# Performance work log

Hardware: AMD Instinct MI355X
Metric: run time of the kernel (lower is better)

Reference implementation:

```python
import jax, jax.numpy as jnp
import numpy as np

E = 8           # num_experts
K = 2           # num_experts_per_tok
D = 1024        # hidden_size
F = 2048        # intermediate_dim
B, S = 1, 2048  # batch, seq_len


def setup_inputs() -> dict:
    key = jax.random.key(0)
    k0, k1, k2, k3, k4, k5 = jax.random.split(key, 6)
    hidden_states = jax.random.normal(k0, (B, S, D), dtype=jnp.float32)
    topk_weights = jax.random.uniform(k1, (B * S, K), dtype=jnp.float32)
    topk_ids = jax.random.randint(k2, (B * S, K), 0, E, dtype=jnp.int32)
    scale = 0.02
    wi_0 = jax.random.normal(k3, (E, D, F), dtype=jnp.float32) * scale
    wi_1 = jax.random.normal(k4, (E, D, F), dtype=jnp.float32) * scale
    wo = jax.random.normal(k5, (E, F, D), dtype=jnp.float32) * scale
    return {"hidden_states": hidden_states, "topk_weights": topk_weights,
            "topk_ids": topk_ids, "wi_0": wi_0, "wi_1": wi_1, "wo": wo}


def _gmm(x, w, group_sizes):
    """Grouped matmul: rows of x are sorted by expert; group_sizes[e] rows use w[e].
    Small fixed loop over experts (E=8); rows not owned by expert e are masked out."""
    n_e = w.shape[0]
    expert_of_row = jnp.repeat(jnp.arange(n_e), group_sizes,
                               total_repeat_length=x.shape[0])  # [M]
    out = jnp.zeros((x.shape[0], w.shape[2]), dtype=x.dtype)
    for e in range(n_e):
        out = out + jnp.where((expert_of_row == e)[:, None], x @ w[e], 0.0)
    return out


def _moe_forward(hidden_states, topk_weights, topk_ids, wi_0, wi_1, wo):
    b, s, d = hidden_states.shape
    k = topk_ids.shape[1]
    n_e = wi_0.shape[0]
    x2d = hidden_states.reshape(b * s, d)

    # ---- permute: sort expanded tokens by selected expert (stable) ----
    flat_experts = jnp.ravel(topk_ids)                       # [T*K]
    sort_idx = jnp.argsort(flat_experts, stable=True)        # [T*K]
    sorted_rows = sort_idx // k                              # source token per row
    x_sorted = jnp.take(x2d, sorted_rows, axis=0)            # [T*K, D]
    group_sizes = jnp.bincount(flat_experts, length=n_e)     # [E]

    # ---- grouped GEMMs with SwiGLU (gate * up, then down) ----
    g0 = _gmm(x_sorted, wi_0, group_sizes)                   # [T*K, F]
    g1 = _gmm(x_sorted, wi_1, group_sizes)                   # [T*K, F]
    h = jax.nn.silu(g0) * g1                                 # fused SiLU-gate
    y = _gmm(h, wo, group_sizes)                             # [T*K, D]

    # ---- unpermute and combine with routing weights (fp32 accum) ----
    unsort_idx = jnp.argsort(sort_idx, stable=True)
    y = jnp.take(y, unsort_idx, axis=0).reshape(b * s, k, d)
    out = jnp.einsum('bke,bk->be', y.astype(jnp.float32),
                     topk_weights.astype(jnp.float32))
    return out.reshape(b, s, d)


def reference(hidden_states, topk_weights, topk_ids, wi_0, wi_1, wo):
    return _moe_forward(hidden_states, topk_weights, topk_ids, wi_0, wi_1, wo)
```

## Files before the change

### kernel.cpp

```cpp
#include <hip/hip_runtime.h>
#include <hip/hip_bf16.h>


#define D_DIM 1024
#define F_DIM 2048
#define ROWS 4096
#define MAXTILE 40
#define LDK 72

using f32x4 = __attribute__((ext_vector_type(4))) float;
using s16x8 = __attribute__((ext_vector_type(8))) short;

__device__ __forceinline__ unsigned pack_trunc(float lo, float hi) {
  return (__float_as_uint(lo) >> 16) | (__float_as_uint(hi) & 0xffff0000u);
}
__device__ __forceinline__ unsigned short bf_rn(float f) {
  unsigned u = __float_as_uint(f);
  u += 0x7fffu + ((u >> 16) & 1u);
  return (unsigned short)(u >> 16);
}

typedef const __attribute__((address_space(1))) void* gp_t;
typedef __attribute__((address_space(3))) void* lp_t;
__device__ __forceinline__ void load16(const void* g, void* l) {
  __builtin_amdgcn_global_load_lds((gp_t)g, (lp_t)l, 16, 0, 0);
}

__global__ __launch_bounds__(512) void route_kernel(const int* __restrict__ ids,
                                                    int* __restrict__ sorted_flat,
                                                    int* __restrict__ tile_meta) {
  __shared__ int cnt[8];
  __shared__ int off[9];
  const int tid = threadIdx.x;
  const int w = tid >> 6, lane = tid & 63;
  int c = 0;
  for (int base = 0; base < ROWS; base += 64) {
    int e = ids[base + lane];
    c += __popcll(__ballot(e == w));
  }
  if (lane == 0) cnt[w] = c;
  __syncthreads();
  if (tid == 0) {
    int o = 0;
    for (int e = 0; e < 8; e++) { off[e] = o; o += cnt[e]; }
    off[8] = o;
    int nT = 0;
    for (int e = 0; e < 8; e++) {
      for (int r0 = off[e]; r0 < off[e + 1]; r0 += 128) {
        tile_meta[1 + 3 * nT] = r0;
        tile_meta[2 + 3 * nT] = off[e + 1];
        tile_meta[3 + 3 * nT] = e;
        nT++;
      }
    }
    tile_meta[0] = nT;
  }
  __syncthreads();
  int pos = off[w];
  const unsigned long long below = (1ull << lane) - 1ull;
  for (int base = 0; base < ROWS; base += 64) {
    int e = ids[base + lane];
    unsigned long long m = __ballot(e == w);
    if (e == w) sorted_flat[pos + __popcll(m & below)] = base + lane;
    pos += __popcll(m);
  }
}

__global__ void zero_kernel(float4* __restrict__ p, int n4) {
  int i = blockIdx.x * blockDim.x + threadIdx.x;
  if (i < n4) p[i] = float4{0.f, 0.f, 0.f, 0.f};
}

__global__ __launch_bounds__(256) void convT_kernel(const float* __restrict__ src,
                                                    unsigned short* __restrict__ dst,
                                                    int Kd, int Nd) {
  __shared__ unsigned short t[64 * 66];
  const int e = blockIdx.z;
  const float* S = src + (size_t)e * Kd * Nd;
  unsigned short* Dp = dst + (size_t)e * Kd * Nd;
  const int n0 = blockIdx.x * 64, k0 = blockIdx.y * 64;
  const int tid = threadIdx.x;
  const int r_ = tid >> 4, c0 = (tid & 15) * 4;
#pragma unroll
  for (int i = 0; i < 4; i++) {
    int r = r_ + i * 16;
    float4 v = *(const float4*)(S + (size_t)(k0 + r) * Nd + n0 + c0);
    t[(c0 + 0) * 66 + r] = bf_rn(v.x);
    t[(c0 + 1) * 66 + r] = bf_rn(v.y);
    t[(c0 + 2) * 66 + r] = bf_rn(v.z);
    t[(c0 + 3) * 66 + r] = bf_rn(v.w);
  }
  __syncthreads();
  const int kb = (tid & 7) * 8;
#pragma unroll
  for (int it = 0; it < 2; it++) {
    int n = (tid >> 3) + it * 32;
    const unsigned* p = (const unsigned*)&t[n * 66 + kb];
    uint4 o = make_uint4(p[0], p[1], p[2], p[3]);
    *(uint4*)(Dp + (size_t)(n0 + n) * Kd + k0 + kb) = o;
  }
}

__global__ __launch_bounds__(256) void gather_kernel(const float* __restrict__ x,
                                                     const int* __restrict__ sorted_flat,
                                                     unsigned short* __restrict__ xs) {
  const int r = blockIdx.x;
  const int tok = sorted_flat[r] >> 1;
  const float4 v = *(const float4*)(x + (size_t)tok * D_DIM + threadIdx.x * 4);
  *(uint2*)(xs + (size_t)r * D_DIM + threadIdx.x * 4) =
      make_uint2((unsigned)bf_rn(v.x) | ((unsigned)bf_rn(v.y) << 16),
                 (unsigned)bf_rn(v.z) | ((unsigned)bf_rn(v.w) << 16));
}

__global__ __launch_bounds__(256, 2) void gemm1_kernel(
    const unsigned short* __restrict__ xs, const unsigned short* __restrict__ w0T,
    const unsigned short* __restrict__ w1T, const int* __restrict__ tile_meta,
    unsigned short* __restrict__ h) {
  __shared__ unsigned short As[128 * 64];
  __shared__ unsigned short B0s[128 * 64];
  __shared__ unsigned short B1s[128 * 64];
  const int tile = blockIdx.x;
  if (tile >= tile_meta[0]) return;
  const int row0 = tile_meta[1 + 3 * tile];
  const int rowEnd = tile_meta[2 + 3 * tile];
  const int e = tile_meta[3 + 3 * tile];
  const int n0 = blockIdx.y * 128;
  const unsigned short* W0 = w0T + ((size_t)e * F_DIM + n0) * D_DIM;
  const unsigned short* W1 = w1T + ((size_t)e * F_DIM + n0) * D_DIM;

  const int tid = threadIdx.x;
  const int lane = tid & 63, wv = tid >> 6;
  const int wm = (wv & 1) * 64, wn = (wv >> 1) * 64;
  const int lm = lane & 15, lq = lane >> 4;

  f32x4 acc0[4][4], acc1[4][4];
#pragma unroll
  for (int i = 0; i < 4; i++)
#pragma unroll
    for (int j = 0; j < 4; j++) { acc0[i][j] = 0.f; acc1[i][j] = 0.f; }

  for (int k0 = 0; k0 < D_DIM; k0 += 64) {
    __syncthreads();
#pragma unroll
    for (int r = 0; r < 4; r++) {
      const int c = r * 4 + wv;
      const int idx = c * 512 + lane * 8;
      const int m = idx >> 6, kk = idx & 63;
      int mc = row0 + m; if (mc > ROWS - 1) mc = ROWS - 1;
      load16(xs + (size_t)mc * D_DIM + k0 + kk, (char*)As + c * 1024);
      load16(W0 + (size_t)m * D_DIM + k0 + kk, (char*)B0s + c * 1024);
      load16(W1 + (size_t)m * D_DIM + k0 + kk, (char*)B1s + c * 1024);
    }
    __syncthreads();
#pragma unroll
    for (int ks = 0; ks < 64; ks += 32) {
      s16x8 af[4], b0[4], b1[4];
#pragma unroll
      for (int t = 0; t < 4; t++) {
        af[t] = *(const s16x8*)&As[(wm + t * 16 + lm) * 64 + ks + lq * 8];
        b0[t] = *(const s16x8*)&B0s[(wn + t * 16 + lm) * 64 + ks + lq * 8];
        b1[t] = *(const s16x8*)&B1s[(wn + t * 16 + lm) * 64 + ks + lq * 8];
      }
#pragma unroll
      for (int im = 0; im < 4; im++)
#pragma unroll
        for (int in = 0; in < 4; in++) {
          acc0[im][in] = __builtin_amdgcn_mfma_f32_16x16x32_bf16(
              af[im], b0[in], acc0[im][in], 0, 0, 0);
          acc1[im][in] = __builtin_amdgcn_mfma_f32_16x16x32_bf16(
              af[im], b1[in], acc1[im][in], 0, 0, 0);
        }
    }
  }
#pragma unroll
  for (int im = 0; im < 4; im++) {
    int gmB = row0 + wm + im * 16 + lq * 4;
#pragma unroll
    for (int in = 0; in < 4; in++) {
      int gn = n0 + wn + in * 16 + lm;
#pragma unroll
      for (int r = 0; r < 4; r++) {
        int gm = gmB + r;
        if (gm < rowEnd) {
          float g = acc0[im][in][r];
          float s = g / (1.f + __expf(-g));
          h[(size_t)gm * F_DIM + gn] = bf_rn(s * acc1[im][in][r]);
        }
      }
    }
  }
}

__global__ __launch_bounds__(256, 3) void gemm2_kernel(
    const unsigned short* __restrict__ h, const unsigned short* __restrict__ woT,
    const float* __restrict__ tw, const int* __restrict__ sorted_flat,
    const int* __restrict__ tile_meta, float* __restrict__ out) {
  __shared__ unsigned short As[128 * 64];
  __shared__ unsigned short Bs[128 * 64];
  __shared__ int sTok[128];
  __shared__ float sWgt[128];
  const int tile = blockIdx.x;
  if (tile >= tile_meta[0]) return;
  const int row0 = tile_meta[1 + 3 * tile];
  const int rowEnd = tile_meta[2 + 3 * tile];
  const int e = tile_meta[3 + 3 * tile];
  const int n0 = blockIdx.y * 128;
  const unsigned short* W = woT + ((size_t)e * D_DIM + n0) * F_DIM;

  const int tid = threadIdx.x;
  if (tid < 128) {
    int r = row0 + tid; if (r > ROWS - 1) r = ROWS - 1;
    int fl = sorted_flat[r];
    sTok[tid] = fl >> 1;
    sWgt[tid] = tw[fl];
  }

  const int lane = tid & 63, wv = tid >> 6;
  const int wm = (wv & 1) * 64, wn = (wv >> 1) * 64;
  const int lm = lane & 15, lq = lane >> 4;

  f32x4 acc[4][4];
#pragma unroll
  for (int i = 0; i < 4; i++)
#pragma unroll
    for (int j = 0; j < 4; j++) acc[i][j] = 0.f;

  for (int k0 = 0; k0 < F_DIM; k0 += 64) {
    __syncthreads();
#pragma unroll
    for (int r = 0; r < 4; r++) {
      const int c = r * 4 + wv;
      const int idx = c * 512 + lane * 8;
      const int m = idx >> 6, kk = idx & 63;
      int mc = row0 + m; if (mc > ROWS - 1) mc = ROWS - 1;
      load16(h + (size_t)mc * F_DIM + k0 + kk, (char*)As + c * 1024);
      load16(W + (size_t)m * F_DIM + k0 + kk, (char*)Bs + c * 1024);
    }
    __syncthreads();
#pragma unroll
    for (int ks = 0; ks < 64; ks += 32) {
      s16x8 af[4], bf[4];
#pragma unroll
      for (int t = 0; t < 4; t++) {
        af[t] = *(const s16x8*)&As[(wm + t * 16 + lm) * 64 + ks + lq * 8];
        bf[t] = *(const s16x8*)&Bs[(wn + t * 16 + lm) * 64 + ks + lq * 8];
      }
#pragma unroll
      for (int im = 0; im < 4; im++)
#pragma unroll
        for (int in = 0; in < 4; in++)
          acc[im][in] = __builtin_amdgcn_mfma_f32_16x16x32_bf16(
              af[im], bf[in], acc[im][in], 0, 0, 0);
    }
  }
#pragma unroll
  for (int im = 0; im < 4; im++) {
    int lrB = wm + im * 16 + lq * 4;
#pragma unroll
    for (int in = 0; in < 4; in++) {
      int gn = n0 + wn + in * 16 + lm;
#pragma unroll
      for (int r = 0; r < 4; r++) {
        int lr = lrB + r;
        int gm = row0 + lr;
        if (gm < rowEnd)
          atomicAdd(out + (size_t)sTok[lr] * D_DIM + gn, sWgt[lr] * acc[im][in][r]);
      }
    }
  }
}

__device__ __forceinline__ void stage_bt(const float* __restrict__ Wt, int ldw,
                                         unsigned short* Bs, int tid) {
#pragma unroll
  for (int it = 0; it < 4; it++) {
    const int kp = (tid & 7) + it * 8;
    const int nq = tid >> 3;
    const float* p = Wt + (size_t)(2 * kp) * ldw + nq * 4;
    const float4 va = *(const float4*)p;
    const float4 vb = *(const float4*)(p + ldw);
    unsigned short* b = Bs + (nq * 4) * LDK + 2 * kp;
    *(unsigned*)(b)           = pack_trunc(va.x, vb.x);
    *(unsigned*)(b + LDK)     = pack_trunc(va.y, vb.y);
    *(unsigned*)(b + 2 * LDK) = pack_trunc(va.z, vb.z);
    *(unsigned*)(b + 3 * LDK) = pack_trunc(va.w, vb.w);
  }
}

__global__ __launch_bounds__(256, 2) void gemm1_fb(
    const float* __restrict__ x, const float* __restrict__ wi0,
    const float* __restrict__ wi1, const int* __restrict__ sorted_flat,
    const int* __restrict__ tile_meta, unsigned short* __restrict__ h) {
  __shared__ unsigned short As[128 * LDK];
  __shared__ unsigned short B0s[128 * LDK];
  __shared__ unsigned short B1s[128 * LDK];
  __shared__ int tok[128];
  const int tile = blockIdx.x;
  if (tile >= tile_meta[0]) return;
  const int row0 = tile_meta[1 + 3 * tile];
  const int rowEnd = tile_meta[2 + 3 * tile];
  const int e = tile_meta[3 + 3 * tile];
  const int n0 = blockIdx.y * 128;
  const float* W0 = wi0 + (size_t)e * D_DIM * F_DIM;
  const float* W1 = wi1 + (size_t)e * D_DIM * F_DIM;
  const int tid = threadIdx.x;
  if (tid < 128) {
    int r = row0 + tid; if (r > ROWS - 1) r = ROWS - 1;
    tok[tid] = sorted_flat[r] >> 1;
  }
  f32x4 acc0[4][4], acc1[4][4];
#pragma unroll
  for (int i = 0; i < 4; i++)
#pragma unroll
    for (int j = 0; j < 4; j++) { acc0[i][j] = 0.f; acc1[i][j] = 0.f; }
  const int lane = tid & 63, wv = tid >> 6;
  const int wm = (wv & 1) * 64, wn = (wv >> 1) * 64;
  const int lm = lane & 15, lq = lane >> 4;
  for (int k0 = 0; k0 < D_DIM; k0 += 64) {
    __syncthreads();
#pragma unroll
    for (int i = 0; i < 8; i++) {
      int idx = tid + i * 256;
      int m = idx >> 4, kq = idx & 15;
      float4 v = *(const float4*)(x + (size_t)tok[m] * D_DIM + k0 + kq * 4);
      *(uint2*)&As[m * LDK + kq * 4] =
          make_uint2(pack_trunc(v.x, v.y), pack_trunc(v.z, v.w));
    }
    stage_bt(W0 + (size_t)k0 * F_DIM + n0, F_DIM, B0s, tid);
    stage_bt(W1 + (size_t)k0 * F_DIM + n0, F_DIM, B1s, tid);
    __syncthreads();
#pragma unroll
    for (int ks = 0; ks < 64; ks += 32) {
      s16x8 af[4], b0[4], b1[4];
#pragma unroll
      for (int t = 0; t < 4; t++) {
        af[t] = *(const s16x8*)&As[(wm + t * 16 + lm) * LDK + ks + lq * 8];
        b0[t] = *(const s16x8*)&B0s[(wn + t * 16 + lm) * LDK + ks + lq * 8];
        b1[t] = *(const s16x8*)&B1s[(wn + t * 16 + lm) * LDK + ks + lq * 8];
      }
#pragma unroll
      for (int im = 0; im < 4; im++)
#pragma unroll
        for (int in = 0; in < 4; in++) {
          acc0[im][in] = __builtin_amdgcn_mfma_f32_16x16x32_bf16(
              af[im], b0[in], acc0[im][in], 0, 0, 0);
          acc1[im][in] = __builtin_amdgcn_mfma_f32_16x16x32_bf16(
              af[im], b1[in], acc1[im][in], 0, 0, 0);
        }
    }
  }
#pragma unroll
  for (int im = 0; im < 4; im++) {
    int gmB = row0 + wm + im * 16 + lq * 4;
#pragma unroll
    for (int in = 0; in < 4; in++) {
      int gn = n0 + wn + in * 16 + lm;
#pragma unroll
      for (int r = 0; r < 4; r++) {
        int gm = gmB + r;
        if (gm < rowEnd) {
          float g = acc0[im][in][r];
          float s = g / (1.f + __expf(-g));
          h[(size_t)gm * F_DIM + gn] = bf_rn(s * acc1[im][in][r]);
        }
      }
    }
  }
}

__global__ __launch_bounds__(256, 3) void gemm2_fb(
    const unsigned short* __restrict__ h, const float* __restrict__ wo,
    const float* __restrict__ tw, const int* __restrict__ sorted_flat,
    const int* __restrict__ tile_meta, float* __restrict__ out) {
  __shared__ unsigned short As[128 * LDK];
  __shared__ unsigned short Bs[128 * LDK];
  __shared__ int sTok[128];
  __shared__ float sWgt[128];
  const int tile = blockIdx.x;
  if (tile >= tile_meta[0]) return;
  const int row0 = tile_meta[1 + 3 * tile];
  const int rowEnd = tile_meta[2 + 3 * tile];
  const int e = tile_meta[3 + 3 * tile];
  const int n0 = blockIdx.y * 128;
  const float* W = wo + (size_t)e * F_DIM * D_DIM;
  const int tid = threadIdx.x;
  if (tid < 128) {
    int r = row0 + tid; if (r > ROWS - 1) r = ROWS - 1;
    int fl = sorted_flat[r];
    sTok[tid] = fl >> 1;
    sWgt[tid] = tw[fl];
  }
  f32x4 acc[4][4];
#pragma unroll
  for (int i = 0; i < 4; i++)
#pragma unroll
    for (int j = 0; j < 4; j++) acc[i][j] = 0.f;
  const int lane = tid & 63, wv = tid >> 6;
  const int wm = (wv & 1) * 64, wn = (wv >> 1) * 64;
  const int lm = lane & 15, lq = lane >> 4;
  for (int k0 = 0; k0 < F_DIM; k0 += 64) {
    __syncthreads();
#pragma unroll
    for (int i = 0; i < 8; i++) {
      int idx = tid + i * 256;
      int m = idx >> 4, kq = idx & 15;
      int gm = row0 + m; if (gm > ROWS - 1) gm = ROWS - 1;
      *(uint2*)&As[m * LDK + kq * 4] =
          *(const uint2*)(h + (size_t)gm * F_DIM + k0 + kq * 4);
    }
    stage_bt(W + (size_t)k0 * D_DIM + n0, D_DIM, Bs, tid);
    __syncthreads();
#pragma unroll
    for (int ks = 0; ks < 64; ks += 32) {
      s16x8 af[4], bf[4];
#pragma unroll
      for (int t = 0; t < 4; t++) {
        af[t] = *(const s16x8*)&As[(wm + t * 16 + lm) * LDK + ks + lq * 8];
        bf[t] = *(const s16x8*)&Bs[(wn + t * 16 + lm) * LDK + ks + lq * 8];
      }
#pragma unroll
      for (int im = 0; im < 4; im++)
#pragma unroll
        for (int in = 0; in < 4; in++)
          acc[im][in] = __builtin_amdgcn_mfma_f32_16x16x32_bf16(
              af[im], bf[in], acc[im][in], 0, 0, 0);
    }
  }
#pragma unroll
  for (int im = 0; im < 4; im++) {
    int lrB = wm + im * 16 + lq * 4;
#pragma unroll
    for (int in = 0; in < 4; in++) {
      int gn = n0 + wn + in * 16 + lm;
#pragma unroll
      for (int r = 0; r < 4; r++) {
        int lr = lrB + r;
        int gm = row0 + lr;
        if (gm < rowEnd)
          atomicAdd(out + (size_t)sTok[lr] * D_DIM + gn, sWgt[lr] * acc[im][in][r]);
      }
    }
  }
}

extern "C" void kernel_launch(void* const* d_in, const int* in_sizes, int n_in,
                              void* d_out, int out_size, void* d_ws, size_t ws_size,
                              hipStream_t stream) {
  const float* x   = (const float*)d_in[0];
  const float* tw  = (const float*)d_in[1];
  const int*   ids = (const int*)d_in[2];
  const float* wi0 = (const float*)d_in[3];
  const float* wi1 = (const float*)d_in[4];
  const float* wo  = (const float*)d_in[5];
  float* out = (float*)d_out;

  int* tile_meta = (int*)d_ws;
  int* sorted_flat = tile_meta + 256;

  const size_t MB = 1024 * 1024;
  const size_t XS_OFF = 32 * 1024;
  const size_t H_OFF  = XS_OFF + 8 * MB;
  const size_t W0_OFF = H_OFF + 16 * MB;
  const size_t W1_OFF = W0_OFF + 32 * MB;
  const size_t WO_OFF = W1_OFF + 32 * MB;
  const size_t NEED   = WO_OFF + 32 * MB;

  route_kernel<<<1, 512, 0, stream>>>(ids, sorted_flat, tile_meta);
  zero_kernel<<<(out_size / 4 + 255) / 256, 256, 0, stream>>>((float4*)out,
                                                              out_size / 4);
  if (ws_size >= NEED) {
    unsigned short* xs  = (unsigned short*)((char*)d_ws + XS_OFF);
    unsigned short* h   = (unsigned short*)((char*)d_ws + H_OFF);
    unsigned short* w0T = (unsigned short*)((char*)d_ws + W0_OFF);
    unsigned short* w1T = (unsigned short*)((char*)d_ws + W1_OFF);
    unsigned short* woT = (unsigned short*)((char*)d_ws + WO_OFF);

    convT_kernel<<<dim3(32, 16, 8), 256, 0, stream>>>(wi0, w0T, D_DIM, F_DIM);
    convT_kernel<<<dim3(32, 16, 8), 256, 0, stream>>>(wi1, w1T, D_DIM, F_DIM);
    convT_kernel<<<dim3(16, 32, 8), 256, 0, stream>>>(wo, woT, F_DIM, D_DIM);
    gather_kernel<<<ROWS, 256, 0, stream>>>(x, sorted_flat, xs);

    dim3 g1(MAXTILE, F_DIM / 128);
    gemm1_kernel<<<g1, 256, 0, stream>>>(xs, w0T, w1T, tile_meta, h);
    dim3 g2(MAXTILE, D_DIM / 128);
    gemm2_kernel<<<g2, 256, 0, stream>>>(h, woT, tw, sorted_flat, tile_meta, out);
  } else {
    unsigned short* h = (unsigned short*)((char*)d_ws + 32768);
    dim3 g1(MAXTILE, F_DIM / 128);
    gemm1_fb<<<g1, 256, 0, stream>>>(x, wi0, wi1, sorted_flat, tile_meta, h);
    dim3 g2(MAXTILE, D_DIM / 128);
    gemm2_fb<<<g2, 256, 0, stream>>>(h, wo, tw, sorted_flat, tile_meta, out);
  }
}
```

Before: 373.0 us.

## Swizzle LDS tiles, fuse weight conversion, replace atomics with separate combine

Merges the three weight transpose/convert kernels into one launch that does register-level transposes without LDS. Adds an XOR swizzle to the LDS layout in both GEMMs to avoid bank conflicts, and raises occupancy hints. gemm2 now uses 64-wide N tiles and writes unweighted rows to a workspace buffer. A new combine kernel gathers each token's two expert outputs via an unsort map and applies the routing weights, which removes the atomics and the zeroing pass. The cost is an extra fp32 intermediate round trip. The y buffer reuses the w0T region, which is safe because gemm1 has finished reading it by then.

Result: slower. 495.2 us (+32.8%).

```diff
diff --git a/kernel.cpp b/kernel.cpp
--- a/kernel.cpp
+++ b/kernel.cpp
@@ -19,6 +19,9 @@
   u += 0x7fffu + ((u >> 16) & 1u);
   return (unsigned short)(u >> 16);
 }
+__device__ __forceinline__ unsigned pack_rn(float lo, float hi) {
+  return (unsigned)bf_rn(lo) | ((unsigned)bf_rn(hi) << 16);
+}
 
 typedef const __attribute__((address_space(1))) void* gp_t;
 typedef __attribute__((address_space(3))) void* lp_t;
@@ -28,6 +31,7 @@
 
 __global__ __launch_bounds__(512) void route_kernel(const int* __restrict__ ids,
                                                     int* __restrict__ sorted_flat,
+                                                    int* __restrict__ unsort,
                                                     int* __restrict__ tile_meta) {
   __shared__ int cnt[8];
   __shared__ int off[9];
@@ -61,7 +65,11 @@
   for (int base = 0; base < ROWS; base += 64) {
     int e = ids[base + lane];
     unsigned long long m = __ballot(e == w);
-    if (e == w) sorted_flat[pos + __popcll(m & below)] = base + lane;
+    if (e == w) {
+      int p = pos + __popcll(m & below);
+      sorted_flat[p] = base + lane;
+      unsort[base + lane] = p;
+    }
     pos += __popcll(m);
   }
 }
@@ -71,33 +79,36 @@
   if (i < n4) p[i] = float4{0.f, 0.f, 0.f, 0.f};
 }
 
-__global__ __launch_bounds__(256) void convT_kernel(const float* __restrict__ src,
-                                                    unsigned short* __restrict__ dst,
-                                                    int Kd, int Nd) {
-  __shared__ unsigned short t[64 * 66];
-  const int e = blockIdx.z;
-  const float* S = src + (size_t)e * Kd * Nd;
-  unsigned short* Dp = dst + (size_t)e * Kd * Nd;
-  const int n0 = blockIdx.x * 64, k0 = blockIdx.y * 64;
-  const int tid = threadIdx.x;
-  const int r_ = tid >> 4, c0 = (tid & 15) * 4;
-#pragma unroll
-  for (int i = 0; i < 4; i++) {
-    int r = r_ + i * 16;
-    float4 v = *(const float4*)(S + (size_t)(k0 + r) * Nd + n0 + c0);
-    t[(c0 + 0) * 66 + r] = bf_rn(v.x);
-    t[(c0 + 1) * 66 + r] = bf_rn(v.y);
-    t[(c0 + 2) * 66 + r] = bf_rn(v.z);
-    t[(c0 + 3) * 66 + r] = bf_rn(v.w);
-  }
-  __syncthreads();
-  const int kb = (tid & 7) * 8;
-#pragma unroll
-  for (int it = 0; it < 2; it++) {
-    int n = (tid >> 3) + it * 32;
-    const unsigned* p = (const unsigned*)&t[n * 66 + kb];
-    uint4 o = make_uint4(p[0], p[1], p[2], p[3]);
-    *(uint4*)(Dp + (size_t)(n0 + n) * Kd + k0 + kb) = o;
+__global__ __launch_bounds__(256) void convT_all(
+    const float* __restrict__ wi0, const float* __restrict__ wi1,
+    const float* __restrict__ wo, unsigned short* __restrict__ w0T,
+    unsigned short* __restrict__ w1T, unsigned short* __restrict__ woT) {
+  const int z = blockIdx.y;
+  const int which = z >> 3, e = z & 7;
+  const float* S;
+  unsigned short* Dp;
+  int Kd, Nd, kb_bits;
+  if (which == 0)      { S = wi0; Dp = w0T; Kd = D_DIM; Nd = F_DIM; kb_bits = 3; }
+  else if (which == 1) { S = wi1; Dp = w1T; Kd = D_DIM; Nd = F_DIM; kb_bits = 3; }
+  else                 { S = wo;  Dp = woT; Kd = F_DIM; Nd = D_DIM; kb_bits = 4; }
+  S  += (size_t)e * Kd * Nd;
+  Dp += (size_t)e * Kd * Nd;
+  const int bx = blockIdx.x;
+  const int k = (bx & ((1 << kb_bits) - 1)) * 128 + (threadIdx.x >> 4) * 8;
+  const int n = (bx >> kb_bits) * 64 + (threadIdx.x & 15) * 4;
+  float4 v[8];
+#pragma unroll
+  for (int i = 0; i < 8; i++)
+    v[i] = *(const float4*)(S + (size_t)(k + i) * Nd + n);
+  const float* fv = (const float*)v;
+#pragma unroll
+  for (int j = 0; j < 4; j++) {
+    uint4 o;
+    o.x = pack_rn(fv[0 * 4 + j], fv[1 * 4 + j]);
+    o.y = pack_rn(fv[2 * 4 + j], fv[3 * 4 + j]);
+    o.z = pack_rn(fv[4 * 4 + j], fv[5 * 4 + j]);
+    o.w = pack_rn(fv[6 * 4 + j], fv[7 * 4 + j]);
+    *(uint4*)(Dp + (size_t)(n + j) * Kd + k) = o;
   }
 }
 
@@ -108,11 +119,14 @@
   const int tok = sorted_flat[r] >> 1;
   const float4 v = *(const float4*)(x + (size_t)tok * D_DIM + threadIdx.x * 4);
   *(uint2*)(xs + (size_t)r * D_DIM + threadIdx.x * 4) =
-      make_uint2((unsigned)bf_rn(v.x) | ((unsigned)bf_rn(v.y) << 16),
-                 (unsigned)bf_rn(v.z) | ((unsigned)bf_rn(v.w) << 16));
-}
-
-__global__ __launch_bounds__(256, 2) void gemm1_kernel(
+      make_uint2(pack_rn(v.x, v.y), pack_rn(v.z, v.w));
+}
+
+__device__ __forceinline__ int sw(int row, int chunk) {
+  return row * 64 + ((chunk ^ (row & 7)) << 3);
+}
+
+__global__ __launch_bounds__(256, 3) void gemm1_kernel(
     const unsigned short* __restrict__ xs, const unsigned short* __restrict__ w0T,
     const unsigned short* __restrict__ w1T, const int* __restrict__ tile_meta,
     unsigned short* __restrict__ h) {
@@ -132,6 +146,8 @@
   const int lane = tid & 63, wv = tid >> 6;
   const int wm = (wv & 1) * 64, wn = (wv >> 1) * 64;
   const int lm = lane & 15, lq = lane >> 4;
+  const int srow = lane >> 3;
+  const int skk = ((lane & 7) ^ srow) << 3;
 
   f32x4 acc0[4][4], acc1[4][4];
 #pragma unroll
@@ -144,22 +160,22 @@
 #pragma unroll
     for (int r = 0; r < 4; r++) {
       const int c = r * 4 + wv;
-      const int idx = c * 512 + lane * 8;
-      const int m = idx >> 6, kk = idx & 63;
+      const int m = c * 8 + srow;
       int mc = row0 + m; if (mc > ROWS - 1) mc = ROWS - 1;
-      load16(xs + (size_t)mc * D_DIM + k0 + kk, (char*)As + c * 1024);
-      load16(W0 + (size_t)m * D_DIM + k0 + kk, (char*)B0s + c * 1024);
-      load16(W1 + (size_t)m * D_DIM + k0 + kk, (char*)B1s + c * 1024);
+      load16(xs + (size_t)mc * D_DIM + k0 + skk, (char*)As + c * 1024);
+      load16(W0 + (size_t)m * D_DIM + k0 + skk, (char*)B0s + c * 1024);
+      load16(W1 + (size_t)m * D_DIM + k0 + skk, (char*)B1s + c * 1024);
     }
     __syncthreads();
 #pragma unroll
     for (int ks = 0; ks < 64; ks += 32) {
+      const int cb = (ks >> 3) + lq;
       s16x8 af[4], b0[4], b1[4];
 #pragma unroll
       for (int t = 0; t < 4; t++) {
-        af[t] = *(const s16x8*)&As[(wm + t * 16 + lm) * 64 + ks + lq * 8];
-        b0[t] = *(const s16x8*)&B0s[(wn + t * 16 + lm) * 64 + ks + lq * 8];
-        b1[t] = *(const s16x8*)&B1s[(wn + t * 16 + lm) * 64 + ks + lq * 8];
+        af[t] = *(const s16x8*)&As[sw(wm + t * 16 + lm, cb)];
+        b0[t] = *(const s16x8*)&B0s[sw(wn + t * 16 + lm, cb)];
+        b1[t] = *(const s16x8*)&B1s[sw(wn + t * 16 + lm, cb)];
       }
 #pragma unroll
       for (int im = 0; im < 4; im++)
@@ -191,83 +207,94 @@
   }
 }
 
-__global__ __launch_bounds__(256, 3) void gemm2_kernel(
+__global__ __launch_bounds__(256, 4) void gemm2_kernel(
     const unsigned short* __restrict__ h, const unsigned short* __restrict__ woT,
-    const float* __restrict__ tw, const int* __restrict__ sorted_flat,
-    const int* __restrict__ tile_meta, float* __restrict__ out) {
+    const int* __restrict__ tile_meta, float* __restrict__ y) {
   __shared__ unsigned short As[128 * 64];
-  __shared__ unsigned short Bs[128 * 64];
-  __shared__ int sTok[128];
-  __shared__ float sWgt[128];
+  __shared__ unsigned short Bs[64 * 64];
   const int tile = blockIdx.x;
   if (tile >= tile_meta[0]) return;
   const int row0 = tile_meta[1 + 3 * tile];
   const int rowEnd = tile_meta[2 + 3 * tile];
   const int e = tile_meta[3 + 3 * tile];
-  const int n0 = blockIdx.y * 128;
+  const int n0 = blockIdx.y * 64;
   const unsigned short* W = woT + ((size_t)e * D_DIM + n0) * F_DIM;
 
   const int tid = threadIdx.x;
-  if (tid < 128) {
-    int r = row0 + tid; if (r > ROWS - 1) r = ROWS - 1;
-    int fl = sorted_flat[r];
-    sTok[tid] = fl >> 1;
-    sWgt[tid] = tw[fl];
-  }
-
   const int lane = tid & 63, wv = tid >> 6;
-  const int wm = (wv & 1) * 64, wn = (wv >> 1) * 64;
+  const int wm = (wv & 1) * 64, wn = (wv >> 1) * 32;
   const int lm = lane & 15, lq = lane >> 4;
-
-  f32x4 acc[4][4];
+  const int srow = lane >> 3;
+  const int skk = ((lane & 7) ^ srow) << 3;
+
+  f32x4 acc[4][2];
 #pragma unroll
   for (int i = 0; i < 4; i++)
 #pragma unroll
-    for (int j = 0; j < 4; j++) acc[i][j] = 0.f;
+    for (int j = 0; j < 2; j++) acc[i][j] = 0.f;
 
   for (int k0 = 0; k0 < F_DIM; k0 += 64) {
     __syncthreads();
 #pragma unroll
     for (int r = 0; r < 4; r++) {
       const int c = r * 4 + wv;
-      const int idx = c * 512 + lane * 8;
-      const int m = idx >> 6, kk = idx & 63;
+      const int m = c * 8 + srow;
       int mc = row0 + m; if (mc > ROWS - 1) mc = ROWS - 1;
-      load16(h + (size_t)mc * F_DIM + k0 + kk, (char*)As + c * 1024);
-      load16(W + (size_t)m * F_DIM + k0 + kk, (char*)Bs + c * 1024);
+      load16(h + (size_t)mc * F_DIM + k0 + skk, (char*)As + c * 1024);
+    }
+#pragma unroll
+    for (int r = 0; r < 2; r++) {
+      const int c = r * 4 + wv;
+      const int m = c * 8 + srow;
+      load16(W + (size_t)m * F_DIM + k0 + skk, (char*)Bs + c * 1024);
     }
     __syncthreads();
 #pragma unroll
     for (int ks = 0; ks < 64; ks += 32) {
-      s16x8 af[4], bf[4];
-#pragma unroll
-      for (int t = 0; t < 4; t++) {
-        af[t] = *(const s16x8*)&As[(wm + t * 16 + lm) * 64 + ks + lq * 8];
-        bf[t] = *(const s16x8*)&Bs[(wn + t * 16 + lm) * 64 + ks + lq * 8];
-      }
+      const int cb = (ks >> 3) + lq;
+      s16x8 af[4], bf[2];
+#pragma unroll
+      for (int t = 0; t < 4; t++)
+        af[t] = *(const s16x8*)&As[sw(wm + t * 16 + lm, cb)];
+#pragma unroll
+      for (int t = 0; t < 2; t++)
+        bf[t] = *(const s16x8*)&Bs[sw(wn + t * 16 + lm, cb)];
 #pragma unroll
       for (int im = 0; im < 4; im++)
 #pragma unroll
-        for (int in = 0; in < 4; in++)
+        for (int in = 0; in < 2; in++)
           acc[im][in] = __builtin_amdgcn_mfma_f32_16x16x32_bf16(
               af[im], bf[in], acc[im][in], 0, 0, 0);
     }
   }
 #pragma unroll
   for (int im = 0; im < 4; im++) {
-    int lrB = wm + im * 16 + lq * 4;
-#pragma unroll
-    for (int in = 0; in < 4; in++) {
+    int gmB = row0 + wm + im * 16 + lq * 4;
+#pragma unroll
+    for (int in = 0; in < 2; in++) {
       int gn = n0 + wn + in * 16 + lm;
 #pragma unroll
       for (int r = 0; r < 4; r++) {
-        int lr = lrB + r;
-        int gm = row0 + lr;
-        if (gm < rowEnd)
-          atomicAdd(out + (size_t)sTok[lr] * D_DIM + gn, sWgt[lr] * acc[im][in][r]);
-      }
-    }
-  }
+        int gm = gmB + r;
+        if (gm < rowEnd) y[(size_t)gm * D_DIM + gn] = acc[im][in][r];
+      }
+    }
+  }
+}
+
+__global__ __launch_bounds__(256) void combine_kernel(const float* __restrict__ y,
+                                                      const float* __restrict__ tw,
+                                                      const int* __restrict__ unsort,
+                                                      float* __restrict__ out) {
+  const int tkn = blockIdx.x;
+  const int r0 = unsort[2 * tkn], r1 = unsort[2 * tkn + 1];
+  const float w0 = tw[2 * tkn], w1 = tw[2 * tkn + 1];
+  const int c = threadIdx.x * 4;
+  float4 a = *(const float4*)(y + (size_t)r0 * D_DIM + c);
+  float4 b = *(const float4*)(y + (size_t)r1 * D_DIM + c);
+  float4 o = {w0 * a.x + w1 * b.x, w0 * a.y + w1 * b.y,
+              w0 * a.z + w1 * b.z, w0 * a.w + w1 * b.w};
+  *(float4*)(out + (size_t)tkn * D_DIM + c) = o;
 }
 
 __device__ __forceinline__ void stage_bt(const float* __restrict__ Wt, int ldw,
@@ -456,39 +483,41 @@
 
   int* tile_meta = (int*)d_ws;
   int* sorted_flat = tile_meta + 256;
+  int* unsort = sorted_flat + ROWS;
 
   const size_t MB = 1024 * 1024;
-  const size_t XS_OFF = 32 * 1024;
+  const size_t XS_OFF = 64 * 1024;
   const size_t H_OFF  = XS_OFF + 8 * MB;
   const size_t W0_OFF = H_OFF + 16 * MB;
   const size_t W1_OFF = W0_OFF + 32 * MB;
   const size_t WO_OFF = W1_OFF + 32 * MB;
   const size_t NEED   = WO_OFF + 32 * MB;
 
-  route_kernel<<<1, 512, 0, stream>>>(ids, sorted_flat, tile_meta);
-  zero_kernel<<<(out_size / 4 + 255) / 256, 256, 0, stream>>>((float4*)out,
-                                                              out_size / 4);
+  route_kernel<<<1, 512, 0, stream>>>(ids, sorted_flat, unsort, tile_meta);
   if (ws_size >= NEED) {
     unsigned short* xs  = (unsigned short*)((char*)d_ws + XS_OFF);
     unsigned short* h   = (unsigned short*)((char*)d_ws + H_OFF);
     unsigned short* w0T = (unsigned short*)((char*)d_ws + W0_OFF);
     unsigned short* w1T = (unsigned short*)((char*)d_ws + W1_OFF);
     unsigned short* woT = (unsigned short*)((char*)d_ws + WO_OFF);
-
-    convT_kernel<<<dim3(32, 16, 8), 256, 0, stream>>>(wi0, w0T, D_DIM, F_DIM);
-    convT_kernel<<<dim3(32, 16, 8), 256, 0, stream>>>(wi1, w1T, D_DIM, F_DIM);
-    convT_kernel<<<dim3(16, 32, 8), 256, 0, stream>>>(wo, woT, F_DIM, D_DIM);
+    float* y = (float*)((char*)d_ws + W0_OFF);
+
+    convT_all<<<dim3(256, 24), 256, 0, stream>>>(wi0, wi1, wo, w0T, w1T, woT);
     gather_kernel<<<ROWS, 256, 0, stream>>>(x, sorted_flat, xs);
-
-    dim3 g1(MAXTILE, F_DIM / 128);
-    gemm1_kernel<<<g1, 256, 0, stream>>>(xs, w0T, w1T, tile_meta, h);
-    dim3 g2(MAXTILE, D_DIM / 128);
-    gemm2_kernel<<<g2, 256, 0, stream>>>(h, woT, tw, sorted_flat, tile_meta, out);
+    gemm1_kernel<<<dim3(MAXTILE, F_DIM / 128), 256, 0, stream>>>(xs, w0T, w1T,
+                                                                 tile_meta, h);
+    gemm2_kernel<<<dim3(MAXTILE, D_DIM / 64), 256, 0, stream>>>(h, woT,
+                                                                tile_meta, y);
+    combine_kernel<<<ROWS / 2, 256, 0, stream>>>(y, tw, unsort, out);
   } else {
-    unsigned short* h = (unsigned short*)((char*)d_ws + 32768);
-    dim3 g1(MAXTILE, F_DIM / 128);
-    gemm1_fb<<<g1, 256, 0, stream>>>(x, wi0, wi1, sorted_flat, tile_meta, h);
-    dim3 g2(MAXTILE, D_DIM / 128);
-    gemm2_fb<<<g2, 256, 0, stream>>>(h, wo, tw, sorted_flat, tile_meta, out);
-  }
-}
+    unsigned short* h = (unsigned short*)((char*)d_ws + XS_OFF);
+    zero_kernel<<<(out_size / 4 + 255) / 256, 256, 0, stream>>>((float4*)out,
+                                                                out_size / 4);
+    gemm1_fb<<<dim3(MAXTILE, F_DIM / 128), 256, 0, stream>>>(x, wi0, wi1,
+                                                             sorted_flat,
+                                                             tile_meta, h);
+    gemm2_fb<<<dim3(MAXTILE, D_DIM / 128), 256, 0, stream>>>(h, wo, tw,
+                                                             sorted_flat,
+                                                             tile_meta, out);
+  }
+}
```
